# Kernel tuning notes

Measured on AMD Instinct MI355X. Metric: run time of the kernel, lower is better.

Reference implementation:

```python
import jax, jax.numpy as jnp
import numpy as np

NUM_GROUPS = 32
EPS = 1e-6


def group_norm(x, gamma, beta):
    # x: [B, C, H, W]
    B, C, H, W = x.shape
    xg = x.reshape(B, NUM_GROUPS, C // NUM_GROUPS, H, W)
    mu = jnp.mean(xg, axis=(2, 3, 4), keepdims=True)
    var = jnp.var(xg, axis=(2, 3, 4), keepdims=True)
    xg = (xg - mu) * jax.lax.rsqrt(var + EPS)
    x = xg.reshape(B, C, H, W)
    return x * gamma[None, :, None, None] + beta[None, :, None, None]


def conv1x1(x, w, b):
    # x: [B, C, H, W], w: [O, C], b: [O]
    return jnp.einsum('bchw,oc->bohw', x, w) + b[None, :, None, None]


def setup_inputs() -> dict:
    key = jax.random.key(0)
    C = 512
    B, H, W = 4, 64, 64
    ks = jax.random.split(key, 10)
    s = 1.0 / np.sqrt(C)
    inp = {
        'x': jax.random.normal(ks[0], (B, C, H, W), dtype=jnp.float32),
        'gamma': jnp.ones((C,), dtype=jnp.float32),
        'beta': jnp.zeros((C,), dtype=jnp.float32),
        'wq': jax.random.normal(ks[1], (C, C), dtype=jnp.float32) * s,
        'bq': jnp.zeros((C,), dtype=jnp.float32),
        'wk': jax.random.normal(ks[2], (C, C), dtype=jnp.float32) * s,
        'bk': jnp.zeros((C,), dtype=jnp.float32),
        'wv': jax.random.normal(ks[3], (C, C), dtype=jnp.float32) * s,
        'bv': jnp.zeros((C,), dtype=jnp.float32),
        'wo': jax.random.normal(ks[4], (C, C), dtype=jnp.float32) * s,
        'bo': jnp.zeros((C,), dtype=jnp.float32),
    }
    return inp


def reference(x, gamma, beta, wq, bq, wk, bk, wv, bv, wo, bo):
    B, C, H, W = x.shape
    h = group_norm(x, gamma, beta)
    q = conv1x1(h, wq, bq).reshape(B, C, H * W)  # [B, C, S]
    k = conv1x1(h, wk, bk).reshape(B, C, H * W)
    v = conv1x1(h, wv, bv).reshape(B, C, H * W)
    scale = C ** (-0.5)
    # scores[b, S, s] = sum_c q[b, c, S] * k[b, c, s]
    w = jnp.einsum('bcS,bcs->bSs', q, k) * scale
    w = jax.nn.softmax(w, axis=-1)
    # out[b, c, S] = sum_s w[b, S, s] * v[b, c, s]
    hattn = jnp.einsum('bSs,bcs->bcS', w, v).reshape(B, C, H, W)
    out = conv1x1(hattn, wo, bo)
    return x + out
```

## Files before the change

### kernel.cpp

```cpp
#include <hip/hip_runtime.h>

#define B_   4
#define C_   512
#define S_   4096
#define G_   32
#define CPG_ 16
#define EPS_ 1e-6f

typedef unsigned short u16;
typedef __bf16 bf16x8 __attribute__((ext_vector_type(8)));
typedef float  f32x4  __attribute__((ext_vector_type(4)));

__device__ __forceinline__ u16 f2bf(float f) {
  unsigned u = __float_as_uint(f);
  u += 0x7fffu + ((u >> 16) & 1u);
  return (u16)(u >> 16);
}
__device__ __forceinline__ float bf2f(u16 h) {
  return __uint_as_float((unsigned)h << 16);
}

__device__ __forceinline__ void g2lds16(const void* g, void* l) {
  __builtin_amdgcn_global_load_lds(
      (const __attribute__((address_space(1))) void*)g,
      (__attribute__((address_space(3))) void*)l, 16, 0, 0);
}

#define BAR()    __builtin_amdgcn_s_barrier()
#define SCHED0() __builtin_amdgcn_sched_barrier(0)
#define WAITV4   asm volatile("s_waitcnt vmcnt(4)" ::: "memory")
#define WAITV0   asm volatile("s_waitcnt vmcnt(0)" ::: "memory")

__device__ __forceinline__ void xcd_swz(int& bx, int& by, int& bz) {
  const int gx = gridDim.x, gy = gridDim.y;
  const int nwg = gx * gy * (int)gridDim.z;
  const int flat = blockIdx.x + gx * (blockIdx.y + gy * blockIdx.z);
  const int q = nwg >> 3;
  const int nf = (flat & 7) * q + (flat >> 3);
  bx = nf % gx;
  const int r = nf / gx;
  by = r % gy;
  bz = r / gy;
}

__global__ __launch_bounds__(256) void f32_to_bf16(const float* __restrict__ in,
                                                   u16* __restrict__ out, int n) {
  int i = blockIdx.x * 256 + threadIdx.x;
  if (i < n) out[i] = f2bf(in[i]);
}

__global__ __launch_bounds__(256) void concat_bias(const float* __restrict__ a,
                                                   const float* __restrict__ b,
                                                   float* __restrict__ o) {
  int i = blockIdx.x * 256 + threadIdx.x;
  o[i] = (i < 512) ? a[i] : b[i - 512];
}

__global__ __launch_bounds__(256) void reduce_l(const float* __restrict__ p,
                                                float* __restrict__ lr) {
  const int i = blockIdx.x * 256 + threadIdx.x;
  const int b = i >> 12, row = i & 4095;
  float s = 0.f;
#pragma unroll
  for (int jb = 0; jb < 16; ++jb) s += p[((size_t)(b * 16 + jb) << 12) + row];
  lr[i] = 1.f / s;
}

__global__ __launch_bounds__(256) void gn_stats(const float* __restrict__ x,
                                                float* __restrict__ stats) {
  const int bg = blockIdx.x;
  const float4* p4 = (const float4*)(x + (size_t)bg * (CPG_ * S_));
  float s = 0.f, ss = 0.f;
  const int tid = threadIdx.x;
  for (int i = tid; i < CPG_ * S_ / 4; i += 256) {
    float4 v = p4[i];
    s  += v.x + v.y + v.z + v.w;
    ss += v.x * v.x + v.y * v.y + v.z * v.z + v.w * v.w;
  }
#pragma unroll
  for (int o = 32; o; o >>= 1) { s += __shfl_xor(s, o, 64); ss += __shfl_xor(ss, o, 64); }
  __shared__ float sm[8];
  const int wid = tid >> 6, lane = tid & 63;
  if (lane == 0) { sm[wid * 2] = s; sm[wid * 2 + 1] = ss; }
  __syncthreads();
  if (tid == 0) {
    s  = sm[0] + sm[2] + sm[4] + sm[6];
    ss = sm[1] + sm[3] + sm[5] + sm[7];
    const float inv = 1.f / (float)(CPG_ * S_);
    float mu = s * inv;
    float var = ss * inv - mu * mu;
    stats[bg * 2]     = mu;
    stats[bg * 2 + 1] = rsqrtf(var + EPS_);
  }
}

__global__ __launch_bounds__(256) void gn_apply_t(const float* __restrict__ x,
                                                  const float* __restrict__ gamma,
                                                  const float* __restrict__ beta,
                                                  const float* __restrict__ stats,
                                                  u16* __restrict__ ht) {
  __shared__ float tile[32][33];
  const int b = blockIdx.z, c0 = blockIdx.y * 32, s0 = blockIdx.x * 32;
  const int tx = threadIdx.x, ty = threadIdx.y;
#pragma unroll
  for (int i = 0; i < 4; ++i) {
    const int c  = c0 + ty + i * 8;
    const float mu = stats[(b * G_ + (c >> 4)) * 2];
    const float rs = stats[(b * G_ + (c >> 4)) * 2 + 1];
    const float v  = x[((size_t)b * C_ + c) * S_ + s0 + tx];
    tile[ty + i * 8][tx] = (v - mu) * rs * gamma[c] + beta[c];
  }
  __syncthreads();
#pragma unroll
  for (int i = 0; i < 4; ++i) {
    const int s = s0 + ty + i * 8;
    ht[((size_t)b * S_ + s) * C_ + c0 + tx] = f2bf(tile[tx][ty + i * 8]);
  }
}

template <int BIAS_MODE, int ZMODE, int SMAX>
__global__ __launch_bounds__(512, 2) void gemm8p(
    const u16* __restrict__ Ag, int lda, long sA,
    const u16* __restrict__ Bg, int ldb, long sB,
    u16* __restrict__ Cg, int ldc, long sC,
    const float* __restrict__ bias, float alpha, int K,
    float* __restrict__ smx) {
  __shared__ u16 As[2][2][8192];
  __shared__ u16 Bs[2][2][8192];
  __shared__ float ps[4][256];
  int bx, by, bz;
  xcd_swz(bx, by, bz);
  const u16 *A, *Bm;
  u16* Cb;
  if (ZMODE == 0) {
    A = Ag + (size_t)bz * sA; Bm = Bg + (size_t)bz * sB; Cb = Cg + (size_t)bz * sC;
  } else {
    const int b = bz >> 1, kh = bz & 1;
    A  = Ag + (size_t)b * 16777216 + (size_t)kh * 2048;
    Bm = Bg + (size_t)b * 4096 + (size_t)kh * 2048;
    Cb = Cg + (size_t)kh * 8388608 + (size_t)b * 2097152;
  }
  const int bm = by * 256, bn = bx * 256;
  const int tid = threadIdx.x;
  const int wid = tid >> 6, lane = tid & 63;
  const int wm = (wid >> 2) * 16, wn = (wid & 3) * 16;
  const int lr = lane & 15, lh = lane >> 4;
  const int x7 = lr & 7;
  const int g0 = (lh ^ x7) * 8, g1 = ((4 | lh) ^ x7) * 8;

  const int sg = (lane & 7) ^ ((lane >> 3) & 7);
  const u16* Abase = A  + (size_t)(bm + wid * 8 + (lane >> 3)) * lda + sg * 8;
  const u16* Bbase = Bm + (size_t)(bn + wid * 8 + (lane >> 3)) * ldb + sg * 8;

#define STGA(D, H, T) do {                                                   \
    const u16* _s = Abase + (size_t)((H) * 128) * lda + (size_t)(T) * 64;    \
    g2lds16(_s,                    &As[D][H][wid * 512]);                    \
    g2lds16(_s + (size_t)64 * lda, &As[D][H][4096 + wid * 512]);             \
  } while (0)
#define STGB(D, H, T) do {                                                   \
    const u16* _s = Bbase + (size_t)((H) * 128) * ldb + (size_t)(T) * 64;    \
    g2lds16(_s,                    &Bs[D][H][wid * 512]);                    \
    g2lds16(_s + (size_t)64 * ldb, &Bs[D][H][4096 + wid * 512]);             \
  } while (0)

  float bias_v[4] = {0.f, 0.f, 0.f, 0.f};
  if (BIAS_MODE == 1) {
#pragma unroll
    for (int g = 0; g < 4; ++g) bias_v[g] = bias[bn + wn + g * 64 + lr];
  }
  SCHED0();

  f32x4 acc[8][4];
  const f32x4 zero = {0.f, 0.f, 0.f, 0.f};
#pragma unroll
  for (int i = 0; i < 8; ++i)
#pragma unroll
    for (int j = 0; j < 4; ++j) acc[i][j] = zero;

  bf16x8 a_[4][2], b_[4][2];

#define RDA(D, AH) do {                                                      \
    _Pragma("unroll") for (int i = 0; i < 4; ++i) {                          \
      const int _o = (wm + i * 32 + lr) * 64;                                \
      a_[i][0] = *(const bf16x8*)&As[D][AH][_o + g0];                        \
      a_[i][1] = *(const bf16x8*)&As[D][AH][_o + g1];                        \
    } } while (0)
#define RDB(D, BH) do {                                                      \
    _Pragma("unroll") for (int j = 0; j < 2; ++j) {                          \
      const int _o = (wn + j * 64 + lr) * 64;                                \
      b_[(BH) * 2 + j][0] = *(const bf16x8*)&Bs[D][BH][_o + g0];             \
      b_[(BH) * 2 + j][1] = *(const bf16x8*)&Bs[D][BH][_o + g1];             \
    } } while (0)
#define MM(AH, BH) do {                                                      \
    __builtin_amdgcn_s_setprio(1);                                           \
    _Pragma("unroll") for (int i = 0; i < 4; ++i)                            \
    _Pragma("unroll") for (int j = 0; j < 2; ++j) {                          \
      acc[(AH) * 4 + i][(BH) * 2 + j] = __builtin_amdgcn_mfma_f32_16x16x32_bf16( \
          a_[i][0], b_[(BH) * 2 + j][0], acc[(AH) * 4 + i][(BH) * 2 + j], 0, 0, 0); \
      acc[(AH) * 4 + i][(BH) * 2 + j] = __builtin_amdgcn_mfma_f32_16x16x32_bf16( \
          a_[i][1], b_[(BH) * 2 + j][1], acc[(AH) * 4 + i][(BH) * 2 + j], 0, 0, 0); \
    }                                                                        \
    __builtin_amdgcn_s_setprio(0);                                           \
  } while (0)

  STGA(0, 0, 0); STGB(0, 1, 0); STGA(0, 1, 0); STGB(0, 0, 0);
  STGA(1, 0, 1); STGB(1, 1, 1);
  WAITV4;
  BAR();

  const int nt = K >> 6;
  for (int i = 0; i < nt / 2; ++i) {
    const int t1 = 2 * i + 1, t2 = 2 * i + 2, t3 = 2 * i + 3;
    const bool s2 = t2 < nt, s3 = t3 < nt;
    RDA(0, 0); RDB(0, 0);
    STGB(1, 0, t1);
    BAR(); MM(0, 0);
    RDB(0, 1);
    STGA(1, 1, t1);
    BAR(); MM(0, 1);
    RDA(0, 1);
    if (s2) STGA(0, 0, t2);
    BAR(); MM(1, 1);
    if (s2) STGB(0, 1, t2);
    if (s2) { WAITV4; } else { WAITV0; }
    BAR(); MM(1, 0);
    RDA(1, 0); RDB(1, 0);
    if (s2) STGA(0, 1, t2);
    BAR(); MM(0, 0);
    RDB(1, 1);
    if (s2) STGB(0, 0, t2);
    BAR(); MM(0, 1);
    RDA(1, 1);
    if (s3) STGA(1, 0, t3);
    BAR(); MM(1, 1);
    if (s3) STGB(1, 1, t3);
    if (s3) { WAITV4; }
    BAR(); MM(1, 0);
  }
#undef STGA
#undef STGB
#undef RDA
#undef RDB
#undef MM
  SCHED0();

  if (SMAX) {
    float rs[8][4];
#pragma unroll
    for (int f = 0; f < 8; ++f) {
      const int row0 = bm + wm + f * 32 + lh * 4;
#pragma unroll
      for (int r = 0; r < 4; ++r) rs[f][r] = 0.f;
#pragma unroll
      for (int g = 0; g < 4; ++g) {
        const int col = bn + wn + g * 64 + lr;
#pragma unroll
        for (int r = 0; r < 4; ++r) {
          const float e = __expf(acc[f][g][r] * alpha);
          rs[f][r] += e;
          Cb[(size_t)(row0 + r) * ldc + col] = f2bf(e);
        }
      }
#pragma unroll
      for (int r = 0; r < 4; ++r) {
        float v = rs[f][r];
        v += __shfl_xor(v, 1, 64);
        v += __shfl_xor(v, 2, 64);
        v += __shfl_xor(v, 4, 64);
        v += __shfl_xor(v, 8, 64);
        rs[f][r] = v;
      }
    }
#pragma unroll
    for (int f = 0; f < 8; ++f)
#pragma unroll
      for (int r = 0; r < 4; ++r)
        if (lr == ((f << 1) | (r >> 1)))
          ps[wid & 3][wm + f * 32 + lh * 4 + r] = rs[f][r];
    __syncthreads();
    if (tid < 256) {
      const float tot = ps[0][tid] + ps[1][tid] + ps[2][tid] + ps[3][tid];
      smx[((size_t)(bz * 16 + bx) << 12) + bm + tid] = tot;
    }
  } else {
#pragma unroll
    for (int f = 0; f < 8; ++f) {
      const int row0 = bm + wm + f * 32 + lh * 4;
#pragma unroll
      for (int g = 0; g < 4; ++g) {
        const int col = bn + wn + g * 64 + lr;
#pragma unroll
        for (int r = 0; r < 4; ++r)
          Cb[(size_t)(row0 + r) * ldc + col] = f2bf(acc[f][g][r] * alpha + bias_v[g]);
      }
    }
  }
}

#define GBM 128
#define GBN 128
#define GBK 64

template <int BIAS_MODE, int OUT_MODE, int BCOMB>
__global__ __launch_bounds__(256) void gemm_abT(
    const u16* __restrict__ Ag, int lda, long sA,
    const u16* __restrict__ Bg, int ldb, long sB,
    void* __restrict__ Cg, int ldc, long sC,
    const float* __restrict__ bias, float alpha,
    const float* __restrict__ xres, const float* __restrict__ lscale,
    const u16* __restrict__ Bg2, int K) {
  __shared__ u16 As[GBM * GBK];
  __shared__ u16 Bs[GBN * GBK];
  const int bz = blockIdx.z;
  const u16* A    = Ag + (size_t)bz * sA;
  const u16* Bmat = Bg + (size_t)bz * sB;
  const int bm = blockIdx.y * GBM, bn = blockIdx.x * GBN;
  const int tid = threadIdx.x;
  const int wid = tid >> 6, lane = tid & 63;
  const int wm = (wid >> 1) * 64, wn = (wid & 1) * 64;
  const int lr = lane & 15, lh = lane >> 4;
  const int srow = lane >> 3, scol = (lane & 7) * 8;

  f32x4 acc[4][4];
  const f32x4 zero = {0.f, 0.f, 0.f, 0.f};
#pragma unroll
  for (int i = 0; i < 4; ++i)
#pragma unroll
    for (int j = 0; j < 4; ++j) acc[i][j] = zero;

  for (int k0 = 0; k0 < K; k0 += GBK) {
    __syncthreads();
#pragma unroll
    for (int i = 0; i < 4; ++i) {
      const int chunk = wid * 4 + i;
      const int row   = chunk * 8 + srow;
      g2lds16(A + (size_t)(bm + row) * lda + (k0 + scol), &As[chunk * 512]);
      if (BCOMB == 0) {
        g2lds16(Bmat + (size_t)(bn + row) * ldb + (k0 + scol), &Bs[chunk * 512]);
      } else {
        const size_t boff = (size_t)(bn + row) * ldb + (k0 + scol);
        const uint4 u0 = *(const uint4*)(Bmat + boff);
        const uint4 u1 = *(const uint4*)(Bg2 + boff);
        const unsigned* p0 = (const unsigned*)&u0;
        const unsigned* p1 = (const unsigned*)&u1;
        unsigned rr[4];
#pragma unroll
        for (int k = 0; k < 4; ++k) {
          const float lo = bf2f((u16)(p0[k] & 0xffffu)) + bf2f((u16)(p1[k] & 0xffffu));
          const float hi = bf2f((u16)(p0[k] >> 16)) + bf2f((u16)(p1[k] >> 16));
          rr[k] = (unsigned)f2bf(lo) | ((unsigned)f2bf(hi) << 16);
        }
        *(uint4*)&Bs[chunk * 512 + lane * 8] = *(const uint4*)rr;
      }
    }
    __syncthreads();
#pragma unroll
    for (int ks = 0; ks < 2; ++ks) {
      bf16x8 a_[4], b_[4];
#pragma unroll
      for (int m = 0; m < 4; ++m)
        a_[m] = *(const bf16x8*)&As[(wm + m * 16 + lr) * GBK + ks * 32 + lh * 8];
#pragma unroll
      for (int n = 0; n < 4; ++n)
        b_[n] = *(const bf16x8*)&Bs[(wn + n * 16 + lr) * GBK + ks * 32 + lh * 8];
#pragma unroll
      for (int m = 0; m < 4; ++m)
#pragma unroll
        for (int n = 0; n < 4; ++n)
          acc[m][n] = __builtin_amdgcn_mfma_f32_16x16x32_bf16(a_[m], b_[n], acc[m][n], 0, 0, 0);
    }
  }

  if (OUT_MODE == 0) {
    u16* Cb = (u16*)Cg + (size_t)bz * sC;
#pragma unroll
    for (int m = 0; m < 4; ++m) {
      const int row0 = bm + wm + m * 16 + lh * 4;
#pragma unroll
      for (int n = 0; n < 4; ++n) {
        const int col = bn + wn + n * 16 + lr;
        float bn_ = (BIAS_MODE == 1) ? bias[col] : 0.f;
#pragma unroll
        for (int r = 0; r < 4; ++r) {
          float bb = (BIAS_MODE == 2) ? bias[row0 + r] : bn_;
          Cb[(size_t)(row0 + r) * ldc + col] = f2bf(acc[m][n][r] * alpha + bb);
        }
      }
    }
  } else {
    float* Ob = (float*)Cg;
#pragma unroll
    for (int m = 0; m < 4; ++m) {
      const int row0 = bm + wm + m * 16 + lh * 4;
#pragma unroll
      for (int n = 0; n < 4; ++n) {
        const int col = bn + wn + n * 16 + lr;
        const int bb = col >> 12, sp = col & (S_ - 1);
        const float lsc = lscale[col];
#pragma unroll
        for (int r = 0; r < 4; ++r) {
          const int o = row0 + r;
          const size_t idx = ((size_t)bb * C_ + o) * S_ + sp;
          Ob[idx] = acc[m][n][r] * lsc + bias[o] + xres[idx];
        }
      }
    }
  }
}

extern "C" void kernel_launch(void* const* d_in, const int* in_sizes, int n_in,
                              void* d_out, int out_size, void* d_ws, size_t ws_size,
                              hipStream_t stream) {
  const float* x     = (const float*)d_in[0];
  const float* gamma = (const float*)d_in[1];
  const float* beta  = (const float*)d_in[2];
  const float* wq = (const float*)d_in[3];
  const float* bq = (const float*)d_in[4];
  const float* wk = (const float*)d_in[5];
  const float* bk = (const float*)d_in[6];
  const float* wv = (const float*)d_in[7];
  const float* bv = (const float*)d_in[8];
  const float* wo = (const float*)d_in[9];
  const float* bo = (const float*)d_in[10];
  float* out = (float*)d_out;

  char* ws = (char*)d_ws;
  float* stats = (float*)ws;
  u16* wqb = (u16*)(ws + 1024);
  u16* wkb = wqb + 262144;
  u16* wvb = wkb + 262144;
  u16* wob = wvb + 262144;
  float* bqk = (float*)(wob + 262144);
  u16* ht  = (u16*)((char*)bqk + 4096);
  u16* qkt = ht + 8388608;
  u16* vv  = qkt + 16777216;
  u16* sc  = vv + 8388608;
  float* partials = (float*)(sc + 67108864);
  float* Lr = partials + 262144;

  f32_to_bf16<<<1024, 256, 0, stream>>>(wq, wqb, 262144);
  f32_to_bf16<<<1024, 256, 0, stream>>>(wk, wkb, 262144);
  f32_to_bf16<<<1024, 256, 0, stream>>>(wv, wvb, 262144);
  f32_to_bf16<<<1024, 256, 0, stream>>>(wo, wob, 262144);
  concat_bias<<<4, 256, 0, stream>>>(bq, bk, bqk);

  gn_stats<<<128, 256, 0, stream>>>(x, stats);
  gn_apply_t<<<dim3(128, 16, 4), dim3(32, 8), 0, stream>>>(x, gamma, beta, stats, ht);

  gemm8p<1, 0, 0><<<dim3(4, 64, 1), 512, 0, stream>>>(ht, 512, 0, wqb, 512, 0,
                                                      qkt, 1024, 0, bqk, 1.f, 512, nullptr);
  gemm_abT<2, 0, 0><<<dim3(128, 4, 1), 256, 0, stream>>>(wvb, 512, 0, ht, 512, 0,
                                                         vv, 16384, 0, bv, 1.f,
                                                         nullptr, nullptr, nullptr, 512);
  gemm8p<0, 0, 1><<<dim3(16, 16, 4), 512, 0, stream>>>(qkt, 1024, 4194304, qkt + 512, 1024, 4194304,
                                                       sc, 4096, 16777216, nullptr,
                                                       0.04419417382415922f, 512, partials);
  reduce_l<<<64, 256, 0, stream>>>(partials, Lr);
  gemm8p<0, 1, 0><<<dim3(2, 16, 8), 512, 0, stream>>>(sc, 4096, 0, vv, 16384, 0,
                                                      qkt, 512, 0, nullptr, 1.f, 2048, nullptr);
  gemm_abT<2, 1, 1><<<dim3(128, 4, 1), 256, 0, stream>>>(wob, 512, 0, qkt, 512, 0,
                                                         out, 0, 0, bo, 1.f,
                                                         x, Lr, qkt + 8388608, 512);
}
```

Before: 287.1 us.

## Switch 256x256 GEMM tile from 16x16x32 to 32x32x16 MFMA

Reworks the main bf16 GEMM kernel to use 32x32x16 MFMA instructions instead of 16x16x32. Each wave now owns 64x32 sub-tiles per half, and the LDS fragment reads, accumulator layout, softmax row-sum reduction and epilogue stores are remapped to match. The larger MFMA shape is meant to cut LDS read traffic per flop and the instruction issue count. In exchange the epilogue store pattern and register use change, which can affect occupancy.

```diff
diff --git a/kernel.cpp b/kernel.cpp
--- a/kernel.cpp
+++ b/kernel.cpp
@@ -10,6 +10,7 @@
 typedef unsigned short u16;
 typedef __bf16 bf16x8 __attribute__((ext_vector_type(8)));
 typedef float  f32x4  __attribute__((ext_vector_type(4)));
+typedef float  f32x16 __attribute__((ext_vector_type(16)));
 
 __device__ __forceinline__ u16 f2bf(float f) {
   unsigned u = __float_as_uint(f);
@@ -143,10 +144,12 @@
   const int bm = by * 256, bn = bx * 256;
   const int tid = threadIdx.x;
   const int wid = tid >> 6, lane = tid & 63;
-  const int wm = (wid >> 2) * 16, wn = (wid & 3) * 16;
-  const int lr = lane & 15, lh = lane >> 4;
-  const int x7 = lr & 7;
-  const int g0 = (lh ^ x7) * 8, g1 = ((4 | lh) ^ x7) * 8;
+  const int gm = wid >> 2, gn = wid & 3;
+  const int l31 = lane & 31, h5 = lane >> 5;
+
+  const int rowA0 = gm * 64 + l31;
+  const int rowA1 = rowA0 + 32;
+  const int rowB  = gn * 32 + l31;
 
   const int sg = (lane & 7) ^ ((lane >> 3) & 7);
   const u16* Abase = A  + (size_t)(bm + wid * 8 + (lane >> 3)) * lda + sg * 8;
@@ -163,42 +166,41 @@
     g2lds16(_s + (size_t)64 * ldb, &Bs[D][H][4096 + wid * 512]);             \
   } while (0)
 
-  float bias_v[4] = {0.f, 0.f, 0.f, 0.f};
+  float bias_v[2] = {0.f, 0.f};
   if (BIAS_MODE == 1) {
 #pragma unroll
-    for (int g = 0; g < 4; ++g) bias_v[g] = bias[bn + wn + g * 64 + lr];
+    for (int bh = 0; bh < 2; ++bh) bias_v[bh] = bias[bn + bh * 128 + gn * 32 + l31];
   }
   SCHED0();
 
-  f32x4 acc[8][4];
-  const f32x4 zero = {0.f, 0.f, 0.f, 0.f};
-#pragma unroll
-  for (int i = 0; i < 8; ++i)
-#pragma unroll
-    for (int j = 0; j < 4; ++j) acc[i][j] = zero;
-
-  bf16x8 a_[4][2], b_[4][2];
-
-#define RDA(D, AH) do {                                                      \
-    _Pragma("unroll") for (int i = 0; i < 4; ++i) {                          \
-      const int _o = (wm + i * 32 + lr) * 64;                                \
-      a_[i][0] = *(const bf16x8*)&As[D][AH][_o + g0];                        \
-      a_[i][1] = *(const bf16x8*)&As[D][AH][_o + g1];                        \
+  f32x16 acc[4][2];
+  const f32x16 zero16 = {0.f, 0.f, 0.f, 0.f, 0.f, 0.f, 0.f, 0.f,
+                         0.f, 0.f, 0.f, 0.f, 0.f, 0.f, 0.f, 0.f};
+#pragma unroll
+  for (int i = 0; i < 4; ++i)
+#pragma unroll
+    for (int j = 0; j < 2; ++j) acc[i][j] = zero16;
+
+  bf16x8 a_[2][4], b0_[4], b1_[4];
+
+#define RDA32(D, AH) do {                                                    \
+    _Pragma("unroll") for (int ks = 0; ks < 4; ++ks) {                       \
+      const int g = ks * 2 + h5;                                             \
+      a_[0][ks] = *(const bf16x8*)&As[D][AH][rowA0 * 64 + ((g ^ (rowA0 & 7)) << 3)]; \
+      a_[1][ks] = *(const bf16x8*)&As[D][AH][rowA1 * 64 + ((g ^ (rowA1 & 7)) << 3)]; \
     } } while (0)
-#define RDB(D, BH) do {                                                      \
-    _Pragma("unroll") for (int j = 0; j < 2; ++j) {                          \
-      const int _o = (wn + j * 64 + lr) * 64;                                \
-      b_[(BH) * 2 + j][0] = *(const bf16x8*)&Bs[D][BH][_o + g0];             \
-      b_[(BH) * 2 + j][1] = *(const bf16x8*)&Bs[D][BH][_o + g1];             \
+#define RDB32(D, BH, BREG) do {                                              \
+    _Pragma("unroll") for (int ks = 0; ks < 4; ++ks) {                       \
+      const int g = ks * 2 + h5;                                             \
+      BREG[ks] = *(const bf16x8*)&Bs[D][BH][rowB * 64 + ((g ^ (rowB & 7)) << 3)]; \
     } } while (0)
-#define MM(AH, BH) do {                                                      \
+#define MM32(AH, BH, BREG) do {                                              \
     __builtin_amdgcn_s_setprio(1);                                           \
-    _Pragma("unroll") for (int i = 0; i < 4; ++i)                            \
-    _Pragma("unroll") for (int j = 0; j < 2; ++j) {                          \
-      acc[(AH) * 4 + i][(BH) * 2 + j] = __builtin_amdgcn_mfma_f32_16x16x32_bf16( \
-          a_[i][0], b_[(BH) * 2 + j][0], acc[(AH) * 4 + i][(BH) * 2 + j], 0, 0, 0); \
-      acc[(AH) * 4 + i][(BH) * 2 + j] = __builtin_amdgcn_mfma_f32_16x16x32_bf16( \
-          a_[i][1], b_[(BH) * 2 + j][1], acc[(AH) * 4 + i][(BH) * 2 + j], 0, 0, 0); \
+    _Pragma("unroll") for (int ks = 0; ks < 4; ++ks) {                       \
+      acc[(AH) * 2 + 0][BH] = __builtin_amdgcn_mfma_f32_32x32x16_bf16(       \
+          a_[0][ks], BREG[ks], acc[(AH) * 2 + 0][BH], 0, 0, 0);              \
+      acc[(AH) * 2 + 1][BH] = __builtin_amdgcn_mfma_f32_32x32x16_bf16(       \
+          a_[1][ks], BREG[ks], acc[(AH) * 2 + 1][BH], 0, 0, 0);              \
     }                                                                        \
     __builtin_amdgcn_s_setprio(0);                                           \
   } while (0)
@@ -212,71 +214,71 @@
   for (int i = 0; i < nt / 2; ++i) {
     const int t1 = 2 * i + 1, t2 = 2 * i + 2, t3 = 2 * i + 3;
     const bool s2 = t2 < nt, s3 = t3 < nt;
-    RDA(0, 0); RDB(0, 0);
+    RDA32(0, 0); RDB32(0, 0, b0_);
     STGB(1, 0, t1);
-    BAR(); MM(0, 0);
-    RDB(0, 1);
+    BAR(); MM32(0, 0, b0_);
+    RDB32(0, 1, b1_);
     STGA(1, 1, t1);
-    BAR(); MM(0, 1);
-    RDA(0, 1);
+    BAR(); MM32(0, 1, b1_);
+    RDA32(0, 1);
     if (s2) STGA(0, 0, t2);
-    BAR(); MM(1, 1);
+    BAR(); MM32(1, 1, b1_);
     if (s2) STGB(0, 1, t2);
     if (s2) { WAITV4; } else { WAITV0; }
-    BAR(); MM(1, 0);
-    RDA(1, 0); RDB(1, 0);
+    BAR(); MM32(1, 0, b0_);
+    RDA32(1, 0); RDB32(1, 0, b0_);
     if (s2) STGA(0, 1, t2);
-    BAR(); MM(0, 0);
-    RDB(1, 1);
+    BAR(); MM32(0, 0, b0_);
+    RDB32(1, 1, b1_);
     if (s2) STGB(0, 0, t2);
-    BAR(); MM(0, 1);
-    RDA(1, 1);
+    BAR(); MM32(0, 1, b1_);
+    RDA32(1, 1);
     if (s3) STGA(1, 0, t3);
-    BAR(); MM(1, 1);
+    BAR(); MM32(1, 1, b1_);
     if (s3) STGB(1, 1, t3);
     if (s3) { WAITV4; }
-    BAR(); MM(1, 0);
+    BAR(); MM32(1, 0, b0_);
   }
 #undef STGA
 #undef STGB
-#undef RDA
-#undef RDB
-#undef MM
+#undef RDA32
+#undef RDB32
+#undef MM32
   SCHED0();
 
   if (SMAX) {
-    float rs[8][4];
-#pragma unroll
-    for (int f = 0; f < 8; ++f) {
-      const int row0 = bm + wm + f * 32 + lh * 4;
-#pragma unroll
-      for (int r = 0; r < 4; ++r) rs[f][r] = 0.f;
-#pragma unroll
-      for (int g = 0; g < 4; ++g) {
-        const int col = bn + wn + g * 64 + lr;
-#pragma unroll
-        for (int r = 0; r < 4; ++r) {
-          const float e = __expf(acc[f][g][r] * alpha);
-          rs[f][r] += e;
-          Cb[(size_t)(row0 + r) * ldc + col] = f2bf(e);
+#pragma unroll
+    for (int AH = 0; AH < 2; ++AH)
+#pragma unroll
+      for (int f = 0; f < 2; ++f) {
+        float rsl[16];
+#pragma unroll
+        for (int r = 0; r < 16; ++r) rsl[r] = 0.f;
+        const int rowbase = bm + AH * 128 + gm * 64 + f * 32;
+#pragma unroll
+        for (int BH = 0; BH < 2; ++BH) {
+          const int colg = bn + BH * 128 + gn * 32 + l31;
+#pragma unroll
+          for (int r = 0; r < 16; ++r) {
+            const int rowg = rowbase + (r & 3) + 8 * (r >> 2) + 4 * h5;
+            const float e = __expf(acc[AH * 2 + f][BH][r] * alpha);
+            rsl[r] += e;
+            Cb[(size_t)rowg * ldc + colg] = f2bf(e);
+          }
+        }
+#pragma unroll
+        for (int r = 0; r < 16; ++r) {
+          float v = rsl[r];
+          v += __shfl_xor(v, 1, 64);
+          v += __shfl_xor(v, 2, 64);
+          v += __shfl_xor(v, 4, 64);
+          v += __shfl_xor(v, 8, 64);
+          v += __shfl_xor(v, 16, 64);
+          const int rr = (r & 3) + 8 * (r >> 2) + 4 * h5;
+          if (l31 == rr)
+            ps[gn][AH * 128 + gm * 64 + f * 32 + rr] = v;
         }
       }
-#pragma unroll
-      for (int r = 0; r < 4; ++r) {
-        float v = rs[f][r];
-        v += __shfl_xor(v, 1, 64);
-        v += __shfl_xor(v, 2, 64);
-        v += __shfl_xor(v, 4, 64);
-        v += __shfl_xor(v, 8, 64);
-        rs[f][r] = v;
-      }
-    }
-#pragma unroll
-    for (int f = 0; f < 8; ++f)
-#pragma unroll
-      for (int r = 0; r < 4; ++r)
-        if (lr == ((f << 1) | (r >> 1)))
-          ps[wid & 3][wm + f * 32 + lh * 4 + r] = rs[f][r];
     __syncthreads();
     if (tid < 256) {
       const float tot = ps[0][tid] + ps[1][tid] + ps[2][tid] + ps[3][tid];
@@ -284,16 +286,21 @@
     }
   } else {
 #pragma unroll
-    for (int f = 0; f < 8; ++f) {
-      const int row0 = bm + wm + f * 32 + lh * 4;
-#pragma unroll
-      for (int g = 0; g < 4; ++g) {
-        const int col = bn + wn + g * 64 + lr;
-#pragma unroll
-        for (int r = 0; r < 4; ++r)
-          Cb[(size_t)(row0 + r) * ldc + col] = f2bf(acc[f][g][r] * alpha + bias_v[g]);
+    for (int AH = 0; AH < 2; ++AH)
+#pragma unroll
+      for (int f = 0; f < 2; ++f) {
+        const int rowbase = bm + AH * 128 + gm * 64 + f * 32;
+#pragma unroll
+        for (int BH = 0; BH < 2; ++BH) {
+          const int colg = bn + BH * 128 + gn * 32 + l31;
+#pragma unroll
+          for (int r = 0; r < 16; ++r) {
+            const int rowg = rowbase + (r & 3) + 8 * (r >> 2) + 4 * h5;
+            Cb[(size_t)rowg * ldc + colg] =
+                f2bf(acc[AH * 2 + f][BH][r] * alpha + bias_v[BH]);
+          }
+        }
       }
-    }
   }
 }
 
```

New measurement: 327.6 us. 1.14x slower.

## Replace split-K P·V GEMM with dedicated 128x128 full-K kernel

Applied to the files above, without the earlier changes.

The P·V product no longer uses the 256x256 gemm8p split into two K halves, whose partial results the output projection had to read and sum. A new 128x128-tile kernel, gemm128pv, runs the full K=4096 with double-buffered LDS and a grid of 4x32x4 blocks, so the output projection reads a single bf16 buffer. This drops the extra partial buffer write, the second read and the rounding in the combine step, at the cost of smaller tiles with less reuse per block and a longer serial K loop.

```diff
diff --git a/kernel.cpp b/kernel.cpp
--- a/kernel.cpp
+++ b/kernel.cpp
@@ -118,7 +118,7 @@
   }
 }
 
-template <int BIAS_MODE, int ZMODE, int SMAX>
+template <int BIAS_MODE, int SMAX>
 __global__ __launch_bounds__(512, 2) void gemm8p(
     const u16* __restrict__ Ag, int lda, long sA,
     const u16* __restrict__ Bg, int ldb, long sB,
@@ -130,16 +130,9 @@
   __shared__ float ps[4][256];
   int bx, by, bz;
   xcd_swz(bx, by, bz);
-  const u16 *A, *Bm;
-  u16* Cb;
-  if (ZMODE == 0) {
-    A = Ag + (size_t)bz * sA; Bm = Bg + (size_t)bz * sB; Cb = Cg + (size_t)bz * sC;
-  } else {
-    const int b = bz >> 1, kh = bz & 1;
-    A  = Ag + (size_t)b * 16777216 + (size_t)kh * 2048;
-    Bm = Bg + (size_t)b * 4096 + (size_t)kh * 2048;
-    Cb = Cg + (size_t)kh * 8388608 + (size_t)b * 2097152;
-  }
+  const u16* A  = Ag + (size_t)bz * sA;
+  const u16* Bm = Bg + (size_t)bz * sB;
+  u16* Cb = Cg + (size_t)bz * sC;
   const int bm = by * 256, bn = bx * 256;
   const int tid = threadIdx.x;
   const int wid = tid >> 6, lane = tid & 63;
@@ -297,18 +290,104 @@
   }
 }
 
+__global__ __launch_bounds__(256, 2) void gemm128pv(
+    const u16* __restrict__ Pg, const u16* __restrict__ Vg,
+    u16* __restrict__ Og, int K) {
+  __shared__ u16 As[2][2][4096];
+  __shared__ u16 Bs[2][2][4096];
+  int bx, by, bz;
+  xcd_swz(bx, by, bz);
+  const u16* A  = Pg + (size_t)bz * 16777216;
+  const u16* Bm = Vg + (size_t)bz * 4096;
+  u16* Cb = Og + (size_t)bz * 2097152;
+  const int bm = by * 128, bn = bx * 128;
+  const int tid = threadIdx.x;
+  const int wid = tid >> 6, lane = tid & 63;
+  const int wm = (wid >> 1) * 64, wn = (wid & 1) * 64;
+  const int AH = wid >> 1, BH = wid & 1;
+  const int lr = lane & 15, lh = lane >> 4;
+  const int x7 = lr & 7;
+  const int g0 = (lh ^ x7) * 8, g1 = ((4 | lh) ^ x7) * 8;
+
+  const int sg = (lane & 7) ^ ((lane >> 3) & 7);
+  const u16* Asrc = A  + (size_t)(bm + wid * 8 + (lane >> 3)) * 4096 + sg * 8;
+  const u16* Bsrc = Bm + (size_t)(bn + wid * 8 + (lane >> 3)) * 16384 + sg * 8;
+
+#define PSTG(D, T) do {                                                      \
+    const size_t _ko = (size_t)(T) * 64;                                     \
+    g2lds16(Asrc + _ko,                        &As[D][0][wid * 512]);        \
+    g2lds16(Asrc + (size_t)32 * 4096 + _ko,    &As[D][0][2048 + wid * 512]); \
+    g2lds16(Asrc + (size_t)64 * 4096 + _ko,    &As[D][1][wid * 512]);        \
+    g2lds16(Asrc + (size_t)96 * 4096 + _ko,    &As[D][1][2048 + wid * 512]); \
+    g2lds16(Bsrc + _ko,                        &Bs[D][0][wid * 512]);        \
+    g2lds16(Bsrc + (size_t)32 * 16384 + _ko,   &Bs[D][0][2048 + wid * 512]); \
+    g2lds16(Bsrc + (size_t)64 * 16384 + _ko,   &Bs[D][1][wid * 512]);        \
+    g2lds16(Bsrc + (size_t)96 * 16384 + _ko,   &Bs[D][1][2048 + wid * 512]); \
+  } while (0)
+
+  f32x4 acc[4][4];
+  const f32x4 zero = {0.f, 0.f, 0.f, 0.f};
+#pragma unroll
+  for (int i = 0; i < 4; ++i)
+#pragma unroll
+    for (int j = 0; j < 4; ++j) acc[i][j] = zero;
+
+  PSTG(0, 0);
+  const int nt = K >> 6;
+  for (int t = 0; t < nt; ++t) {
+    const int d = t & 1;
+    WAITV0;
+    BAR();
+    if (t + 1 < nt) PSTG(d ^ 1, t + 1);
+    bf16x8 a0_[4], a1_[4], b0_[4], b1_[4];
+#pragma unroll
+    for (int m = 0; m < 4; ++m) {
+      const int ro = (m * 16 + lr) * 64;
+      a0_[m] = *(const bf16x8*)&As[d][AH][ro + g0];
+      a1_[m] = *(const bf16x8*)&As[d][AH][ro + g1];
+      b0_[m] = *(const bf16x8*)&Bs[d][BH][ro + g0];
+      b1_[m] = *(const bf16x8*)&Bs[d][BH][ro + g1];
+    }
+    __builtin_amdgcn_s_setprio(1);
+#pragma unroll
+    for (int m = 0; m < 4; ++m)
+#pragma unroll
+      for (int n = 0; n < 4; ++n)
+        acc[m][n] = __builtin_amdgcn_mfma_f32_16x16x32_bf16(a0_[m], b0_[n], acc[m][n], 0, 0, 0);
+#pragma unroll
+    for (int m = 0; m < 4; ++m)
+#pragma unroll
+      for (int n = 0; n < 4; ++n)
+        acc[m][n] = __builtin_amdgcn_mfma_f32_16x16x32_bf16(a1_[m], b1_[n], acc[m][n], 0, 0, 0);
+    __builtin_amdgcn_s_setprio(0);
+  }
+#undef PSTG
+  SCHED0();
+
+#pragma unroll
+  for (int m = 0; m < 4; ++m) {
+    const int row0 = bm + wm + m * 16 + lh * 4;
+#pragma unroll
+    for (int n = 0; n < 4; ++n) {
+      const int col = bn + wn + n * 16 + lr;
+#pragma unroll
+      for (int r = 0; r < 4; ++r)
+        Cb[(size_t)(row0 + r) * 512 + col] = f2bf(acc[m][n][r]);
+    }
+  }
+}
+
 #define GBM 128
 #define GBN 128
 #define GBK 64
 
-template <int BIAS_MODE, int OUT_MODE, int BCOMB>
+template <int BIAS_MODE, int OUT_MODE>
 __global__ __launch_bounds__(256) void gemm_abT(
     const u16* __restrict__ Ag, int lda, long sA,
     const u16* __restrict__ Bg, int ldb, long sB,
     void* __restrict__ Cg, int ldc, long sC,
     const float* __restrict__ bias, float alpha,
-    const float* __restrict__ xres, const float* __restrict__ lscale,
-    const u16* __restrict__ Bg2, int K) {
+    const float* __restrict__ xres, const float* __restrict__ lscale, int K) {
   __shared__ u16 As[GBM * GBK];
   __shared__ u16 Bs[GBN * GBK];
   const int bz = blockIdx.z;
@@ -334,24 +413,8 @@
     for (int i = 0; i < 4; ++i) {
       const int chunk = wid * 4 + i;
       const int row   = chunk * 8 + srow;
-      g2lds16(A + (size_t)(bm + row) * lda + (k0 + scol), &As[chunk * 512]);
-      if (BCOMB == 0) {
-        g2lds16(Bmat + (size_t)(bn + row) * ldb + (k0 + scol), &Bs[chunk * 512]);
-      } else {
-        const size_t boff = (size_t)(bn + row) * ldb + (k0 + scol);
-        const uint4 u0 = *(const uint4*)(Bmat + boff);
-        const uint4 u1 = *(const uint4*)(Bg2 + boff);
-        const unsigned* p0 = (const unsigned*)&u0;
-        const unsigned* p1 = (const unsigned*)&u1;
-        unsigned rr[4];
-#pragma unroll
-        for (int k = 0; k < 4; ++k) {
-          const float lo = bf2f((u16)(p0[k] & 0xffffu)) + bf2f((u16)(p1[k] & 0xffffu));
-          const float hi = bf2f((u16)(p0[k] >> 16)) + bf2f((u16)(p1[k] >> 16));
-          rr[k] = (unsigned)f2bf(lo) | ((unsigned)f2bf(hi) << 16);
-        }
-        *(uint4*)&Bs[chunk * 512 + lane * 8] = *(const uint4*)rr;
-      }
+      g2lds16(A    + (size_t)(bm + row) * lda + (k0 + scol), &As[chunk * 512]);
+      g2lds16(Bmat + (size_t)(bn + row) * ldb + (k0 + scol), &Bs[chunk * 512]);
     }
     __syncthreads();
 #pragma unroll
@@ -447,18 +510,17 @@
   gn_stats<<<128, 256, 0, stream>>>(x, stats);
   gn_apply_t<<<dim3(128, 16, 4), dim3(32, 8), 0, stream>>>(x, gamma, beta, stats, ht);
 
-  gemm8p<1, 0, 0><<<dim3(4, 64, 1), 512, 0, stream>>>(ht, 512, 0, wqb, 512, 0,
-                                                      qkt, 1024, 0, bqk, 1.f, 512, nullptr);
-  gemm_abT<2, 0, 0><<<dim3(128, 4, 1), 256, 0, stream>>>(wvb, 512, 0, ht, 512, 0,
-                                                         vv, 16384, 0, bv, 1.f,
-                                                         nullptr, nullptr, nullptr, 512);
-  gemm8p<0, 0, 1><<<dim3(16, 16, 4), 512, 0, stream>>>(qkt, 1024, 4194304, qkt + 512, 1024, 4194304,
-                                                       sc, 4096, 16777216, nullptr,
-                                                       0.04419417382415922f, 512, partials);
+  gemm8p<1, 0><<<dim3(4, 64, 1), 512, 0, stream>>>(ht, 512, 0, wqb, 512, 0,
+                                                   qkt, 1024, 0, bqk, 1.f, 512, nullptr);
+  gemm_abT<2, 0><<<dim3(128, 4, 1), 256, 0, stream>>>(wvb, 512, 0, ht, 512, 0,
+                                                      vv, 16384, 0, bv, 1.f,
+                                                      nullptr, nullptr, 512);
+  gemm8p<0, 1><<<dim3(16, 16, 4), 512, 0, stream>>>(qkt, 1024, 4194304, qkt + 512, 1024, 4194304,
+                                                    sc, 4096, 16777216, nullptr,
+                                                    0.04419417382415922f, 512, partials);
   reduce_l<<<64, 256, 0, stream>>>(partials, Lr);
-  gemm8p<0, 1, 0><<<dim3(2, 16, 8), 512, 0, stream>>>(sc, 4096, 0, vv, 16384, 0,
-                                                      qkt, 512, 0, nullptr, 1.f, 2048, nullptr);
-  gemm_abT<2, 1, 1><<<dim3(128, 4, 1), 256, 0, stream>>>(wob, 512, 0, qkt, 512, 0,
-                                                         out, 0, 0, bo, 1.f,
-                                                         x, Lr, qkt + 8388608, 512);
-}
+  gemm128pv<<<dim3(4, 32, 4), 256, 0, stream>>>(sc, vv, qkt, 4096);
+  gemm_abT<2, 1><<<dim3(128, 4, 1), 256, 0, stream>>>(wob, 512, 0, qkt, 512, 0,
+                                                      out, 0, 0, bo, 1.f,
+                                                      x, Lr, 512);
+}
```

Measured after the change: 296.2 us. +3.2%, slower.
